# Performance work log

Measured on AMD Instinct MI355X. Metric: run time of the kernel, lower is better.

Reference implementation:

```python
import jax, jax.numpy as jnp
import numpy as np

N, E, F_IN, E_IN, H, L, C = 50000, 500000, 128, 16, 128, 2, 2
BN_EPS = 1e-5


def _linear_params(key, fan_in, fan_out):
    k1, k2 = jax.random.split(key)
    w = jax.random.normal(k1, (fan_in, fan_out), jnp.float32) * (1.0 / np.sqrt(fan_in))
    b = jax.random.normal(k2, (fan_out,), jnp.float32) * 0.01
    return w, b


def setup_inputs() -> dict:
    key = jax.random.key(0)
    ks = jax.random.split(key, 32)
    x = jax.random.normal(ks[0], (N, F_IN), jnp.float32)
    edge_attr = jax.random.normal(ks[1], (E, E_IN), jnp.float32)
    edge_index = jax.random.randint(ks[2], (2, E), 0, N, jnp.int64)

    node_w, node_b = _linear_params(ks[3], F_IN, H)
    edge_w, edge_b = _linear_params(ks[4], E_IN, H)

    def stack(fn, base):
        ws, bs = zip(*[fn(jax.random.fold_in(ks[base], i)) for i in range(L)])
        return jnp.stack(ws), jnp.stack(bs)

    conv_w1, conv_b1 = stack(lambda k: _linear_params(k, H, H), 5)
    conv_w2, conv_b2 = stack(lambda k: _linear_params(k, H, H), 6)
    emlp_w1, emlp_b1 = stack(lambda k: _linear_params(k, 3 * H, H), 7)
    emlp_w2, emlp_b2 = stack(lambda k: _linear_params(k, H, H), 8)
    bn_gamma = jnp.ones((L, H), jnp.float32)
    bn_beta = jnp.zeros((L, H), jnp.float32)

    mlp_w1, mlp_b1 = _linear_params(ks[9], 3 * H, 50)
    mlp_w2, mlp_b2 = _linear_params(ks[10], 50, 25)
    mlp_w3, mlp_b3 = _linear_params(ks[11], 25, C)

    return dict(x=x, edge_attr=edge_attr,
                node_w=node_w, node_b=node_b, edge_w=edge_w, edge_b=edge_b,
                conv_w1=conv_w1, conv_b1=conv_b1, conv_w2=conv_w2, conv_b2=conv_b2,
                bn_gamma=bn_gamma, bn_beta=bn_beta,
                emlp_w1=emlp_w1, emlp_b1=emlp_b1, emlp_w2=emlp_w2, emlp_b2=emlp_b2,
                mlp_w1=mlp_w1, mlp_b1=mlp_b1, mlp_w2=mlp_w2, mlp_b2=mlp_b2,
                mlp_w3=mlp_w3, mlp_b3=mlp_b3, edge_index=edge_index)


def _forward(x, edge_attr, node_w, node_b, edge_w, edge_b,
             conv_w1, conv_b1, conv_w2, conv_b2, bn_gamma, bn_beta,
             emlp_w1, emlp_b1, emlp_w2, emlp_b2,
             mlp_w1, mlp_b1, mlp_w2, mlp_b2, mlp_w3, mlp_b3, edge_index):
    src, dst = edge_index[0], edge_index[1]
    h = x @ node_w + node_b                      # [N, H]
    ea = edge_attr @ edge_w + edge_b             # [E, H]
    for i in range(L):
        # GINEConv: message = relu(x_src + edge_attr), scatter-add at dst
        msg = jax.nn.relu(h[src] + ea)           # [E, H]
        agg = jax.ops.segment_sum(msg, dst, num_segments=N)
        z = h + agg                              # eps = 0
        z = jax.nn.relu(z @ conv_w1[i] + conv_b1[i]) @ conv_w2[i] + conv_b2[i]
        # BatchNorm (training-mode batch statistics over nodes)
        mu = jnp.mean(z, axis=0)
        var = jnp.var(z, axis=0)
        z = bn_gamma[i] * (z - mu) * jax.lax.rsqrt(var + BN_EPS) + bn_beta[i]
        h = (h + jax.nn.relu(z)) * 0.5
        # edge update MLP
        eu = jnp.concatenate([h[src], h[dst], ea], axis=-1)  # [E, 3H]
        ea = ea + (jax.nn.relu(eu @ emlp_w1[i] + emlp_b1[i]) @ emlp_w2[i] + emlp_b2[i]) * 0.5
    # readout: x[edge_index.T].reshape(-1, 2H) cat edge_attr -> [E, 3H]
    feat = jnp.concatenate([h[src], h[dst], ea], axis=-1)
    o = jax.nn.relu(feat @ mlp_w1 + mlp_b1)      # dropout is eval no-op
    o = jax.nn.relu(o @ mlp_w2 + mlp_b2)
    return o @ mlp_w3 + mlp_b3                   # [E, n_classes]


def reference(x, edge_attr, node_w, node_b, edge_w, edge_b,
              conv_w1, conv_b1, conv_w2, conv_b2, bn_gamma, bn_beta,
              emlp_w1, emlp_b1, emlp_w2, emlp_b2,
              mlp_w1, mlp_b1, mlp_w2, mlp_b2, mlp_w3, mlp_b3, edge_index):
    return _forward(x, edge_attr, node_w, node_b, edge_w, edge_b,
                    conv_w1, conv_b1, conv_w2, conv_b2, bn_gamma, bn_beta,
                    emlp_w1, emlp_b1, emlp_w2, emlp_b2,
                    mlp_w1, mlp_b1, mlp_w2, mlp_b2, mlp_w3, mlp_b3, edge_index)
```

## Files before the change

kernel.cpp:

```cpp
#include <hip/hip_runtime.h>


#define NN 50000
#define NE 500000
#define HD 128

typedef _Float16 f16;
typedef _Float16 f16x8 __attribute__((ext_vector_type(8)));
typedef _Float16 f16x4 __attribute__((ext_vector_type(4)));
typedef _Float16 f16x2 __attribute__((ext_vector_type(2)));
typedef float f32x4 __attribute__((ext_vector_type(4)));
typedef unsigned short ushort_t;

#define MFMA16(a, b, c) __builtin_amdgcn_mfma_f32_16x16x32_f16((a), (b), (c), 0, 0, 0)

#define P_NODE_W 0
#define P_NODE_B 16384
#define P_EDGE_W 16512
#define P_EDGE_B 18560
#define P_CONV_W1 18688
#define P_CONV_B1 51456
#define P_CONV_W2 51712
#define P_CONV_B2 84480
#define P_GAMMA 84736
#define P_BETA 84992
#define P_EMLP_W1 85248
#define P_EMLP_B1 183552
#define P_EMLP_W2 183808
#define P_EMLP_B2 216576
#define P_MLP_W1 216832
#define P_MLP_B1 236032
#define P_MLP_W2 236082
#define P_MLP_B2 237332
#define P_MLP_W3 237357
#define P_MLP_B3 237407
#define P_TOTAL 237409

__device__ __forceinline__ float bf2f(unsigned short u) {
    union { unsigned int i; float f; } v;
    v.i = ((unsigned int)u) << 16;
    return v.f;
}

__global__ __launch_bounds__(256) void k_detect(
    const unsigned int* nw, const int* ei, int* flags) {
    __shared__ int cF, cI;
    if (threadIdx.x == 0) { cF = 0; cI = 0; }
    __syncthreads();
    unsigned int u = nw[threadIdx.x];
    int e = (int)((u >> 7) & 0xFFu);
    int odd = ei[2 * threadIdx.x + 1];
    if (e >= 100 && e <= 140) atomicAdd(&cF, 1);
    if (odd != 0) atomicAdd(&cI, 1);
    __syncthreads();
    if (threadIdx.x == 0) {
        flags[0] = (cF < 160) ? 1 : 0;
        flags[1] = (cI < 64) ? 1 : 0;
    }
}

__global__ __launch_bounds__(256) void k_cvt(
    const void* src, f16* dst, int n4, const int* flags) {
    int i = blockIdx.x * 256 + threadIdx.x;
    if (i >= n4) return;
    f16x4 o;
    if (flags[0]) {
        float4 v = ((const float4*)src)[i];
        o[0] = (f16)v.x; o[1] = (f16)v.y; o[2] = (f16)v.z; o[3] = (f16)v.w;
    } else {
        ushort4 v = ((const ushort4*)src)[i];
        o[0] = (f16)bf2f(v.x); o[1] = (f16)bf2f(v.y);
        o[2] = (f16)bf2f(v.z); o[3] = (f16)bf2f(v.w);
    }
    ((f16x4*)dst)[i] = o;
}

__global__ __launch_bounds__(256) void k_cvt_prm(
    const void* p0, const void* p1, const void* p2, const void* p3,
    const void* p4, const void* p5, const void* p6, const void* p7,
    const void* p8, const void* p9, const void* p10, const void* p11,
    const void* p12, const void* p13, const void* p14, const void* p15,
    const void* p16, const void* p17, const void* p18, const void* p19,
    float* prm, const int* flags) {
    int i = blockIdx.x * 256 + threadIdx.x;
    if (i >= P_TOTAL) return;
    const int offs[21] = {P_NODE_W, P_NODE_B, P_EDGE_W, P_EDGE_B, P_CONV_W1,
                          P_CONV_B1, P_CONV_W2, P_CONV_B2, P_GAMMA, P_BETA,
                          P_EMLP_W1, P_EMLP_B1, P_EMLP_W2, P_EMLP_B2, P_MLP_W1,
                          P_MLP_B1, P_MLP_W2, P_MLP_B2, P_MLP_W3, P_MLP_B3,
                          P_TOTAL};
    const void* srcs[20] = {p0, p1, p2, p3, p4, p5, p6, p7, p8, p9, p10, p11,
                            p12, p13, p14, p15, p16, p17, p18, p19};
    int s = 0;
#pragma unroll
    for (int k = 1; k < 20; ++k)
        if (i >= offs[k]) s = k;
    int li = i - offs[s];
    float v = flags[0] ? ((const float*)srcs[s])[li]
                       : bf2f(((const ushort_t*)srcs[s])[li]);
    prm[i] = v;
}

__global__ __launch_bounds__(256) void k_cvt_idx(
    const int* src, int* dst, const int* flags) {
    int i = blockIdx.x * 256 + threadIdx.x;
    if (i >= 2 * NE) return;
    dst[i] = flags[1] ? src[2 * i] : src[i];
}

__global__ __launch_bounds__(256) void k_hist(const int* eix, int* cnt) {
    int e = blockIdx.x * 256 + threadIdx.x;
    if (e < NE) atomicAdd(&cnt[eix[NE + e]], 1);
}

__global__ __launch_bounds__(256) void k_scanA(const int* cnt, int* bsum) {
    __shared__ int wsum[4];
    int tid = threadIdx.x;
    int i = blockIdx.x * 256 + tid;
    int v = (i < NN) ? cnt[i] : 0;
#pragma unroll
    for (int s = 1; s < 64; s <<= 1) v += __shfl_xor(v, s);
    if ((tid & 63) == 0) wsum[tid >> 6] = v;
    __syncthreads();
    if (tid == 0) bsum[blockIdx.x] = wsum[0] + wsum[1] + wsum[2] + wsum[3];
}

__global__ __launch_bounds__(256) void k_scanB(const int* bsum, int* bpre, int* off) {
    __shared__ int l[200];
    int tid = threadIdx.x;
    if (tid < 196) l[tid] = bsum[tid];
    __syncthreads();
    if (tid == 0) {
        int run = 0;
        for (int b = 0; b < 196; ++b) { int t = l[b]; l[b] = run; run += t; }
        off[NN] = run;
    }
    __syncthreads();
    if (tid < 196) bpre[tid] = l[tid];
}

__global__ __launch_bounds__(256) void k_scanC(
    const int* cnt, const int* bpre, int* off, int* cursor) {
    __shared__ int wsum[4];
    int tid = threadIdx.x;
    int lane = tid & 63, wave = tid >> 6;
    int i = blockIdx.x * 256 + tid;
    int v = (i < NN) ? cnt[i] : 0;
    int incl = v;
#pragma unroll
    for (int s = 1; s < 64; s <<= 1) {
        int t = __shfl_up(incl, s);
        if (lane >= s) incl += t;
    }
    if (lane == 63) wsum[wave] = incl;
    __syncthreads();
    int add = bpre[blockIdx.x];
    for (int w = 0; w < 4; ++w)
        if (w < wave) add += wsum[w];
    int excl = add + incl - v;
    if (i < NN) { off[i] = excl; cursor[i] = excl; }
}

__global__ __launch_bounds__(256) void k_scatter(
    const int* eix, int* cursor, int* eord) {
    int e = blockIdx.x * 256 + threadIdx.x;
    if (e >= NE) return;
    int d = eix[NE + e];
    int pos = atomicAdd(&cursor[d], 1);
    eord[pos] = e;
}

__global__ __launch_bounds__(256) void k_gidx(
    const int* eix, const int* eord, int* ssrc, int* sdst) {
    int i = blockIdx.x * 256 + threadIdx.x;
    if (i >= NE) return;
    int e = eord[i];
    ssrc[i] = eix[e];
    sdst[i] = eix[NE + e];
}

__global__ __launch_bounds__(256) void k_agg(
    const f16* ea, const f16* h16, const int* ssrc, const int* off, f16* agg16) {
    int wid = (blockIdx.x * 256 + threadIdx.x) >> 6;
    int lane = threadIdx.x & 63;
    int beg = off[wid], end = off[wid + 1];
    float a0 = 0.f, a1 = 0.f;
    for (int i = beg; i < end; ++i) {
        int s = ssrc[i];
        f16x2 ev = *(const f16x2*)(ea + (size_t)i * HD + lane * 2);
        f16x2 hv = *(const f16x2*)(h16 + (size_t)s * HD + lane * 2);
        a0 += fmaxf((float)ev[0] + (float)hv[0], 0.f);
        a1 += fmaxf((float)ev[1] + (float)hv[1], 0.f);
    }
    f16x2 o; o[0] = (f16)a0; o[1] = (f16)a1;
    *(f16x2*)(agg16 + (size_t)wid * HD + lane * 2) = o;
}

__global__ __launch_bounds__(256) void k_prep(const float* prm, f16* wbuf) {
    int gid = blockIdx.x * 256 + threadIdx.x;
    if (gid < 13 * 16384) {
        int seg = gid >> 14;
        int idx = gid & 16383;
        int off;
        switch (seg) {
            case 0: off = P_NODE_W; break;
            case 1: off = P_CONV_W1; break;
            case 2: off = P_CONV_W1 + 16384; break;
            case 3: off = P_CONV_W2; break;
            case 4: off = P_CONV_W2 + 16384; break;
            case 5: case 6: case 7: off = P_EMLP_W1 + (seg - 5) * 16384; break;
            case 8: case 9: case 10: off = P_EMLP_W1 + 49152 + (seg - 8) * 16384; break;
            case 11: off = P_EMLP_W2; break;
            default: off = P_EMLP_W2 + 16384; break;
        }
        int fb = idx >> 9;
        int sub = (idx & 511) >> 3;
        int j = idx & 7;
        int q = sub >> 4, n = sub & 15;
        int nt = fb >> 2, kt = fb & 3;
        int k = kt * 32 + q * 8 + j;
        int c = nt * 16 + n;
        wbuf[gid] = (f16)prm[off + k * 128 + c];
    } else {
        int t = gid - 13 * 16384;
        if (t >= 3 * 8192) return;
        int s = t >> 13;
        int idx = t & 8191;
        int fb = idx >> 9;
        int sub = (idx & 511) >> 3;
        int j = idx & 7;
        int q = sub >> 4, n = sub & 15;
        int nt = fb >> 2, kt = fb & 3;
        int k = s * 128 + kt * 32 + q * 8 + j;
        int c = nt * 16 + n;
        float v = (c < 50) ? prm[P_MLP_W1 + k * 50 + c] : 0.f;
        wbuf[13 * 16384 + s * 8192 + idx] = (f16)v;
    }
}

__global__ __launch_bounds__(256) void k_node_lin(
    const f16* xc, const f16* wT, const float* bias, f16* h_f16) {
    __shared__ __align__(16) f16 wlds[16384];
    int tid = threadIdx.x;
    {
        const uint4* s = (const uint4*)wT;
        uint4* d = (uint4*)wlds;
        for (int i = tid; i < 2048; i += 256) d[i] = s[i];
    }
    __syncthreads();
    int wave = tid >> 6, lane = tid & 63, q = lane >> 4, ln = lane & 15;
    int rowbase = blockIdx.x * 128 + wave * 32;
    f32x4 acc[2][8] = {};
#pragma unroll
    for (int kt = 0; kt < 4; ++kt) {
        int koff = kt * 32 + q * 8;
        f16x8 a[2];
#pragma unroll
        for (int mt = 0; mt < 2; ++mt) {
            int row = min(rowbase + mt * 16 + ln, NN - 1);
            a[mt] = *(const f16x8*)(xc + row * HD + koff);
        }
#pragma unroll
        for (int nt = 0; nt < 8; ++nt) {
            f16x8 b = *(const f16x8*)&wlds[(nt * 4 + kt) * 512 + lane * 8];
            acc[0][nt] = MFMA16(a[0], b, acc[0][nt]);
            acc[1][nt] = MFMA16(a[1], b, acc[1][nt]);
        }
    }
#pragma unroll
    for (int nt = 0; nt < 8; ++nt) {
        int col = nt * 16 + ln;
        float bv = bias[col];
#pragma unroll
        for (int mt = 0; mt < 2; ++mt)
#pragma unroll
            for (int r = 0; r < 4; ++r) {
                int row = rowbase + mt * 16 + q * 4 + r;
                if (row < NN) h_f16[row * HD + col] = (f16)(acc[mt][nt][r] + bv);
            }
    }
}

__global__ __launch_bounds__(256) void k_edge_lin(
    const f16* eattr, const float* ew, const float* ebias, const int* eord,
    f16* ea) {
    __shared__ float wl[16 * 128];
    __shared__ float bl[128];
    __shared__ float al[64 * 16];
    int tid = threadIdx.x;
    int eb = blockIdx.x * 64;
    for (int i = tid; i < 2048; i += 256) wl[i] = ew[i];
    if (tid < 128) bl[tid] = ebias[tid];
    {
        int e_l = tid >> 2, k0 = (tid & 3) * 4;
        int er = eord[min(eb + e_l, NE - 1)];
        f16x4 u = *(const f16x4*)(eattr + er * 16 + k0);
        al[e_l * 16 + k0 + 0] = (float)u[0];
        al[e_l * 16 + k0 + 1] = (float)u[1];
        al[e_l * 16 + k0 + 2] = (float)u[2];
        al[e_l * 16 + k0 + 3] = (float)u[3];
    }
    __syncthreads();
    for (int i = 0; i < 32; ++i) {
        int o = i * 256 + tid;
        int e_l = o >> 7, c = o & 127;
        float s = bl[c];
#pragma unroll
        for (int k = 0; k < 16; ++k) s += al[e_l * 16 + k] * wl[k * 128 + c];
        int e = eb + e_l;
        if (e < NE) ea[(size_t)e * HD + c] = (f16)s;
    }
}

__global__ __launch_bounds__(256) void k_conv1(
    const f16* h16, const f16* agg16, const f16* wT, const float* bias,
    f16* t_node) {
    __shared__ __align__(16) f16 wlds[16384];
    int tid = threadIdx.x;
    {
        const uint4* s = (const uint4*)wT;
        uint4* d = (uint4*)wlds;
        for (int i = tid; i < 2048; i += 256) d[i] = s[i];
    }
    __syncthreads();
    int wave = tid >> 6, lane = tid & 63, q = lane >> 4, ln = lane & 15;
    int rowbase = blockIdx.x * 128 + wave * 32;
    f32x4 acc[2][8] = {};
#pragma unroll
    for (int kt = 0; kt < 4; ++kt) {
        int koff = kt * 32 + q * 8;
        f16x8 a[2];
#pragma unroll
        for (int mt = 0; mt < 2; ++mt) {
            int row = min(rowbase + mt * 16 + ln, NN - 1);
            f16x8 hv = *(const f16x8*)(h16 + row * HD + koff);
            f16x8 gv = *(const f16x8*)(agg16 + row * HD + koff);
            f16x8 av;
#pragma unroll
            for (int j = 0; j < 8; ++j) av[j] = (f16)((float)hv[j] + (float)gv[j]);
            a[mt] = av;
        }
#pragma unroll
        for (int nt = 0; nt < 8; ++nt) {
            f16x8 b = *(const f16x8*)&wlds[(nt * 4 + kt) * 512 + lane * 8];
            acc[0][nt] = MFMA16(a[0], b, acc[0][nt]);
            acc[1][nt] = MFMA16(a[1], b, acc[1][nt]);
        }
    }
#pragma unroll
    for (int nt = 0; nt < 8; ++nt) {
        int col = nt * 16 + ln;
        float bv = bias[col];
#pragma unroll
        for (int mt = 0; mt < 2; ++mt)
#pragma unroll
            for (int r = 0; r < 4; ++r) {
                int row = rowbase + mt * 16 + q * 4 + r;
                if (row < NN)
                    t_node[row * HD + col] = (f16)fmaxf(acc[mt][nt][r] + bv, 0.f);
            }
    }
}

__global__ __launch_bounds__(256) void k_conv2(
    const f16* t_node, const f16* wT, const float* bias, f16* z2, float* stats) {
    __shared__ __align__(16) f16 wlds[16384];
    int tid = threadIdx.x;
    {
        const uint4* s = (const uint4*)wT;
        uint4* d = (uint4*)wlds;
        for (int i = tid; i < 2048; i += 256) d[i] = s[i];
    }
    __syncthreads();
    int wave = tid >> 6, lane = tid & 63, q = lane >> 4, ln = lane & 15;
    int rowbase = blockIdx.x * 128 + wave * 32;
    f32x4 acc[2][8] = {};
#pragma unroll
    for (int kt = 0; kt < 4; ++kt) {
        int koff = kt * 32 + q * 8;
        f16x8 a[2];
#pragma unroll
        for (int mt = 0; mt < 2; ++mt) {
            int row = min(rowbase + mt * 16 + ln, NN - 1);
            a[mt] = *(const f16x8*)(t_node + row * HD + koff);
        }
#pragma unroll
        for (int nt = 0; nt < 8; ++nt) {
            f16x8 b = *(const f16x8*)&wlds[(nt * 4 + kt) * 512 + lane * 8];
            acc[0][nt] = MFMA16(a[0], b, acc[0][nt]);
            acc[1][nt] = MFMA16(a[1], b, acc[1][nt]);
        }
    }
#pragma unroll
    for (int nt = 0; nt < 8; ++nt) {
        int col = nt * 16 + ln;
        float bv = bias[col];
        float s = 0.f, s2 = 0.f;
#pragma unroll
        for (int mt = 0; mt < 2; ++mt)
#pragma unroll
            for (int r = 0; r < 4; ++r) {
                int row = rowbase + mt * 16 + q * 4 + r;
                if (row < NN) {
                    float v = acc[mt][nt][r] + bv;
                    z2[row * HD + col] = (f16)v;
                    s += v;
                    s2 += v * v;
                }
            }
        s += __shfl_xor(s, 16);  s += __shfl_xor(s, 32);
        s2 += __shfl_xor(s2, 16); s2 += __shfl_xor(s2, 32);
        if (lane < 16) {
            atomicAdd(&stats[col], s);
            atomicAdd(&stats[HD + col], s2);
        }
    }
}

__global__ __launch_bounds__(256) void k_bn(
    const f16* z2, const float* stats, const float* gamma, const float* beta,
    f16* h16) {
    int gid = blockIdx.x * 256 + threadIdx.x;
    if (gid >= NN * HD / 4) return;
    int base = gid * 4;
    int c0 = base & (HD - 1);
    f16x4 z = *(const f16x4*)(z2 + base);
    f16x4 h = *(const f16x4*)(h16 + base);
    f16x4 ho;
#pragma unroll
    for (int j = 0; j < 4; ++j) {
        int c = c0 + j;
        float mu = stats[c] * (1.0f / NN);
        float var = stats[HD + c] * (1.0f / NN) - mu * mu;
        float zn = gamma[c] * ((float)z[j] - mu) * rsqrtf(var + 1e-5f) + beta[c];
        ho[j] = (f16)(((float)h[j] + fmaxf(zn, 0.f)) * 0.5f);
    }
    *(f16x4*)(h16 + base) = ho;
}

__global__ __launch_bounds__(256, 4) void k_emlp(
    const f16* h16, const int* ssrc, const int* sdst, const f16* w1T,
    const float* b1, const f16* w2T, const float* b2, f16* ea) {
    __shared__ __align__(16) f16 wlds[16384];
    int tid = threadIdx.x;
    int eb = blockIdx.x * 128;
    int wave = tid >> 6, lane = tid & 63, q = lane >> 4, ln = lane & 15;
    int g0 = min(eb + wave * 32 + ln, NE - 1);
    int g1 = min(eb + wave * 32 + 16 + ln, NE - 1);
    int is0 = ssrc[g0], is1 = ssrc[g1];
    int id0 = sdst[g0], id1 = sdst[g1];
    f32x4 acc[2][8] = {};
    for (int seg = 0; seg < 3; ++seg) {
        __syncthreads();
        {
            const uint4* s = (const uint4*)(w1T + seg * 16384);
            uint4* d = (uint4*)wlds;
            for (int i = tid; i < 2048; i += 256) d[i] = s[i];
        }
        __syncthreads();
        const f16 *p0, *p1;
        if (seg == 0) {
            p0 = h16 + (size_t)is0 * HD;
            p1 = h16 + (size_t)is1 * HD;
        } else if (seg == 1) {
            p0 = h16 + (size_t)id0 * HD;
            p1 = h16 + (size_t)id1 * HD;
        } else {
            p0 = ea + (size_t)g0 * HD;
            p1 = ea + (size_t)g1 * HD;
        }
        f16x8 f0[4], f1[4];
#pragma unroll
        for (int kt = 0; kt < 4; ++kt) {
            f0[kt] = *(const f16x8*)(p0 + kt * 32 + q * 8);
            f1[kt] = *(const f16x8*)(p1 + kt * 32 + q * 8);
        }
#pragma unroll
        for (int kt = 0; kt < 4; ++kt)
#pragma unroll
            for (int mt = 0; mt < 8; ++mt) {
                f16x8 a = *(const f16x8*)&wlds[(mt * 4 + kt) * 512 + lane * 8];
                acc[0][mt] = MFMA16(a, f0[kt], acc[0][mt]);
                acc[1][mt] = MFMA16(a, f1[kt], acc[1][mt]);
            }
    }
    union HU { f16 h; unsigned short u; };
    unsigned int pk[2][4][4];
#pragma unroll
    for (int ntl = 0; ntl < 2; ++ntl)
#pragma unroll
        for (int kt = 0; kt < 4; ++kt) {
            f32x4 blo = *(const f32x4*)(b1 + (2 * kt) * 16 + q * 4);
            f32x4 bhi = *(const f32x4*)(b1 + (2 * kt + 1) * 16 + q * 4);
#pragma unroll
            for (int r = 0; r < 4; ++r) {
                HU lo, hi;
                lo.h = (f16)fmaxf(acc[ntl][2 * kt][r] + blo[r], 0.f);
                hi.h = (f16)fmaxf(acc[ntl][2 * kt + 1][r] + bhi[r], 0.f);
                pk[ntl][kt][r] =
                    (unsigned int)lo.u | ((unsigned int)hi.u << 16);
            }
        }
    __syncthreads();
    {
        const uint4* s = (const uint4*)w2T;
        uint4* d = (uint4*)wlds;
        for (int i = tid; i < 2048; i += 256) d[i] = s[i];
    }
    __syncthreads();
    int s1 = (((2 * q) & 3) << 4) | ln;
    int s2 = (((2 * q + 1) & 3) << 4) | ln;
    int hsh = (q >> 1) * 16;
    f32x4 acc2[2][8] = {};
#pragma unroll
    for (int kt = 0; kt < 4; ++kt) {
        f16x8 bf[2];
#pragma unroll
        for (int ntl = 0; ntl < 2; ++ntl) {
            union { unsigned short u[8]; f16x8 v; } bb;
#pragma unroll
            for (int r = 0; r < 4; ++r) {
                unsigned int v1 = (unsigned int)__shfl((int)pk[ntl][kt][r], s1);
                unsigned int v2 = (unsigned int)__shfl((int)pk[ntl][kt][r], s2);
                bb.u[r] = (unsigned short)(v1 >> hsh);
                bb.u[4 + r] = (unsigned short)(v2 >> hsh);
            }
            bf[ntl] = bb.v;
        }
#pragma unroll
        for (int mt = 0; mt < 8; ++mt) {
            f16x8 a = *(const f16x8*)&wlds[(mt * 4 + kt) * 512 + lane * 8];
            acc2[0][mt] = MFMA16(a, bf[0], acc2[0][mt]);
            acc2[1][mt] = MFMA16(a, bf[1], acc2[1][mt]);
        }
    }
#pragma unroll
    for (int ntl = 0; ntl < 2; ++ntl) {
        int e = eb + wave * 32 + ntl * 16 + ln;
        if (e < NE) {
            f16* erow = ea + (size_t)e * HD;
#pragma unroll
            for (int mt = 0; mt < 8; ++mt) {
                int c0 = mt * 16 + q * 4;
                f32x4 bv = *(const f32x4*)(b2 + c0);
                f16x4 old = *(const f16x4*)(erow + c0);
                f16x4 nw;
#pragma unroll
                for (int r = 0; r < 4; ++r)
                    nw[r] = (f16)((float)old[r] +
                                  0.5f * (acc2[ntl][mt][r] + bv[r]));
                *(f16x4*)(erow + c0) = nw;
            }
        }
    }
}

__global__ __launch_bounds__(256) void k_readout(
    const f16* h16, const f16* ea, const int* ssrc, const int* sdst,
    const int* eord, const f16* w1Tp, const float* mb1, const float* mw2,
    const float* mb2, const float* mw3, const float* mb3, float* out) {
    __shared__ __align__(16) f16 wlds[8192];
    __shared__ f16 o1[256 * 58];
    __shared__ float w2l[50 * 28];
    __shared__ float w3l[50];
    __shared__ float b2l[25];
    __shared__ float b3l[2];
    __shared__ int sidx[256], didx[256];
    int tid = threadIdx.x;
    int eb = blockIdx.x * 256;
    {
        int e = min(eb + tid, NE - 1);
        sidx[tid] = ssrc[e];
        didx[tid] = sdst[e];
    }
    for (int i = tid; i < 50 * 28; i += 256) {
        int k = i / 28, ko = i - k * 28;
        w2l[i] = (ko < 25) ? mw2[k * 25 + ko] : 0.f;
    }
    if (tid < 50) w3l[tid] = mw3[tid];
    if (tid < 25) b2l[tid] = mb2[tid];
    if (tid < 2) b3l[tid] = mb3[tid];
    int wave = tid >> 6, lane = tid & 63, q = lane >> 4, ln = lane & 15;
    f32x4 acc[4][4] = {};
    for (int seg = 0; seg < 3; ++seg) {
        __syncthreads();
        {
            const uint4* s = (const uint4*)(w1Tp + seg * 8192);
            uint4* d = (uint4*)wlds;
            for (int i = tid; i < 1024; i += 256) d[i] = s[i];
        }
        __syncthreads();
#pragma unroll
        for (int kt = 0; kt < 4; ++kt) {
            int koff = kt * 32 + q * 8;
            f16x8 a[4];
#pragma unroll
            for (int mt = 0; mt < 4; ++mt) {
                int le = wave * 64 + mt * 16 + ln;
                const f16* ap;
                if (seg == 0)      ap = h16 + (size_t)sidx[le] * HD + koff;
                else if (seg == 1) ap = h16 + (size_t)didx[le] * HD + koff;
                else               ap = ea + (size_t)min(eb + le, NE - 1) * HD + koff;
                a[mt] = *(const f16x8*)ap;
            }
#pragma unroll
            for (int nt = 0; nt < 4; ++nt) {
                f16x8 b = *(const f16x8*)&wlds[(nt * 4 + kt) * 512 + lane * 8];
#pragma unroll
                for (int mt = 0; mt < 4; ++mt)
                    acc[mt][nt] = MFMA16(a[mt], b, acc[mt][nt]);
            }
        }
    }
#pragma unroll
    for (int nt = 0; nt < 4; ++nt) {
        int col = nt * 16 + ln;
        if (col < 50) {
            float bv = mb1[col];
#pragma unroll
            for (int mt = 0; mt < 4; ++mt)
#pragma unroll
                for (int r = 0; r < 4; ++r) {
                    int le = wave * 64 + mt * 16 + q * 4 + r;
                    o1[le * 58 + col] = (f16)fmaxf(acc[mt][nt][r] + bv, 0.f);
                }
        }
    }
    __syncthreads();
    float o2[25];
#pragma unroll
    for (int ko = 0; ko < 25; ++ko) o2[ko] = b2l[ko];
    for (int k = 0; k < 50; ++k) {
        float a = (float)o1[tid * 58 + k];
#pragma unroll
        for (int ko = 0; ko < 25; ++ko) o2[ko] += a * w2l[k * 28 + ko];
    }
    float r0 = b3l[0], r1 = b3l[1];
#pragma unroll
    for (int ko = 0; ko < 25; ++ko) {
        float a = fmaxf(o2[ko], 0.f);
        r0 += a * w3l[ko * 2];
        r1 += a * w3l[ko * 2 + 1];
    }
    int e = eb + tid;
    if (e < NE) {
        int oe = eord[e];
        float2 o; o.x = r0; o.y = r1;
        *(float2*)(out + (size_t)oe * 2) = o;
    }
}

extern "C" void kernel_launch(void* const* d_in, const int* in_sizes, int n_in,
                              void* d_out, int out_size, void* d_ws, size_t ws_size,
                              hipStream_t stream) {
    const size_t WS_NEED = 197425936ULL;
    if (ws_size < WS_NEED) {
        hipMemsetAsync(d_out, 0, (size_t)out_size * 4, stream);
        return;
    }
    char* ws = (char*)d_ws;
    f16* ea = (f16*)(ws);
    f16* hf16 = (f16*)(ws + 128000000LL);
    f16* agg16 = (f16*)(ws + 140800000LL);
    f16* xc = (f16*)(ws + 140800000LL);
    int* eord = (int*)(ws + 153600000LL);
    int* off = (int*)(ws + 155600000LL);
    int* cntcur = (int*)(ws + 155800064LL);
    int* bsum = (int*)(ws + 156000064LL);
    int* bpre = (int*)(ws + 156001088LL);
    int* ssrc = (int*)(ws + 156002176LL);
    int* sdst = (int*)(ws + 158002176LL);
    f16* eattr16 = (f16*)(ws + 166400000LL);
    f16* z2 = (f16*)(ws + 166400000LL);
    f16* tn = (f16*)(ws + 179200000LL);
    f16* wbuf = (f16*)(ws + 192000000LL);
    float* stats = (float*)(ws + 192475136LL);
    float* prm = (float*)(ws + 192476160LL);
    int* eix = (int*)(ws + 193425920LL);
    int* flags = (int*)(ws + 197425920LL);
    float* out = (float*)d_out;

    k_detect<<<1, 256, 0, stream>>>((const unsigned int*)d_in[2],
                                    (const int*)d_in[22], flags);
    k_cvt<<<6250, 256, 0, stream>>>(d_in[0], xc, 1600000, flags);
    k_cvt<<<7813, 256, 0, stream>>>(d_in[1], eattr16, 2000000, flags);
    k_cvt_prm<<<928, 256, 0, stream>>>(
        d_in[2], d_in[3], d_in[4], d_in[5], d_in[6], d_in[7], d_in[8], d_in[9],
        d_in[10], d_in[11], d_in[12], d_in[13], d_in[14], d_in[15], d_in[16],
        d_in[17], d_in[18], d_in[19], d_in[20], d_in[21], prm, flags);
    k_cvt_idx<<<3907, 256, 0, stream>>>((const int*)d_in[22], eix, flags);

    hipMemsetAsync(cntcur, 0, NN * 4, stream);
    k_hist<<<1954, 256, 0, stream>>>(eix, cntcur);
    k_scanA<<<196, 256, 0, stream>>>(cntcur, bsum);
    k_scanB<<<1, 256, 0, stream>>>(bsum, bpre, off);
    k_scanC<<<196, 256, 0, stream>>>(cntcur, bpre, off, cntcur);
    k_scatter<<<1954, 256, 0, stream>>>(eix, cntcur, eord);
    k_gidx<<<1954, 256, 0, stream>>>(eix, eord, ssrc, sdst);

    k_prep<<<928, 256, 0, stream>>>(prm, wbuf);
    k_node_lin<<<391, 256, 0, stream>>>(xc, wbuf, prm + P_NODE_B, hf16);
    k_edge_lin<<<7813, 256, 0, stream>>>(eattr16, prm + P_EDGE_W, prm + P_EDGE_B,
                                         eord, ea);

    for (int l = 0; l < 2; ++l) {
        hipMemsetAsync(stats, 0, 1024, stream);
        k_agg<<<12500, 256, 0, stream>>>(ea, hf16, ssrc, off, agg16);
        k_conv1<<<391, 256, 0, stream>>>(hf16, agg16, wbuf + (1 + l) * 16384,
                                         prm + P_CONV_B1 + l * HD, tn);
        k_conv2<<<391, 256, 0, stream>>>(tn, wbuf + (3 + l) * 16384,
                                         prm + P_CONV_B2 + l * HD, z2, stats);
        k_bn<<<6250, 256, 0, stream>>>(z2, stats, prm + P_GAMMA + l * HD,
                                       prm + P_BETA + l * HD, hf16);
        k_emlp<<<3907, 256, 0, stream>>>(hf16, ssrc, sdst,
                                         wbuf + (5 + l * 3) * 16384,
                                         prm + P_EMLP_B1 + l * HD,
                                         wbuf + (11 + l) * 16384,
                                         prm + P_EMLP_B2 + l * HD, ea);
    }
    k_readout<<<1954, 256, 0, stream>>>(hf16, ea, ssrc, sdst, eord,
                                        wbuf + 13 * 16384,
                                        prm + P_MLP_B1, prm + P_MLP_W2,
                                        prm + P_MLP_B2, prm + P_MLP_W3,
                                        prm + P_MLP_B3, out);
}
```

Baseline: 966.4 us.

## Make edge MLP kernel persistent with all weights resident in LDS

Changes k_emlp to a persistent kernel with 256 blocks of 1024 threads. Each block loads both layer weight matrices (128 KB of f16) into shared memory once, then each wave loops over 32-edge tiles. This removes the repeated per-block weight staging and the __syncthreads barriers between segments. The cost is one 1024-thread block per CU, since 128 KB of LDS leaves little room for more, and waves get no cross-block latency hiding for the gathered loads.

```diff
diff --git a/kernel.cpp b/kernel.cpp
--- a/kernel.cpp
+++ b/kernel.cpp
@@ -438,118 +438,120 @@
     *(f16x4*)(h16 + base) = ho;
 }
 
-__global__ __launch_bounds__(256, 4) void k_emlp(
-    const f16* h16, const int* ssrc, const int* sdst, const f16* w1T,
-    const float* b1, const f16* w2T, const float* b2, f16* ea) {
-    __shared__ __align__(16) f16 wlds[16384];
-    int tid = threadIdx.x;
-    int eb = blockIdx.x * 128;
+__global__ __launch_bounds__(1024, 4) void k_emlp(
+    const f16* __restrict__ h16, const int* __restrict__ ssrc,
+    const int* __restrict__ sdst, const f16* __restrict__ w1T,
+    const float* __restrict__ b1, const f16* __restrict__ w2T,
+    const float* __restrict__ b2, f16* __restrict__ ea) {
+    __shared__ __align__(16) f16 wlds[65536];
+    int tid = threadIdx.x;
+    {
+        const uint4* s1 = (const uint4*)w1T;
+        uint4* d = (uint4*)wlds;
+        for (int i = tid; i < 6144; i += 1024) d[i] = s1[i];
+        const uint4* s2 = (const uint4*)w2T;
+        uint4* d2 = (uint4*)(wlds + 49152);
+        for (int i = tid; i < 2048; i += 1024) d2[i] = s2[i];
+    }
+    __syncthreads();
     int wave = tid >> 6, lane = tid & 63, q = lane >> 4, ln = lane & 15;
-    int g0 = min(eb + wave * 32 + ln, NE - 1);
-    int g1 = min(eb + wave * 32 + 16 + ln, NE - 1);
-    int is0 = ssrc[g0], is1 = ssrc[g1];
-    int id0 = sdst[g0], id1 = sdst[g1];
-    f32x4 acc[2][8] = {};
-    for (int seg = 0; seg < 3; ++seg) {
-        __syncthreads();
-        {
-            const uint4* s = (const uint4*)(w1T + seg * 16384);
-            uint4* d = (uint4*)wlds;
-            for (int i = tid; i < 2048; i += 256) d[i] = s[i];
-        }
-        __syncthreads();
-        const f16 *p0, *p1;
-        if (seg == 0) {
-            p0 = h16 + (size_t)is0 * HD;
-            p1 = h16 + (size_t)is1 * HD;
-        } else if (seg == 1) {
-            p0 = h16 + (size_t)id0 * HD;
-            p1 = h16 + (size_t)id1 * HD;
-        } else {
-            p0 = ea + (size_t)g0 * HD;
-            p1 = ea + (size_t)g1 * HD;
-        }
-        f16x8 f0[4], f1[4];
+    int sh1 = (((2 * q) & 3) << 4) | ln;
+    int sh2 = (((2 * q + 1) & 3) << 4) | ln;
+    int hsh = (q >> 1) * 16;
+    const int NT = (NE + 31) / 32;
+    for (int t = blockIdx.x * 16 + wave; t < NT; t += 256 * 16) {
+        int eb32 = t * 32;
+        int g0 = min(eb32 + ln, NE - 1);
+        int g1 = min(eb32 + 16 + ln, NE - 1);
+        int is0 = ssrc[g0], is1 = ssrc[g1];
+        int id0 = sdst[g0], id1 = sdst[g1];
+        f32x4 acc[2][8] = {};
+#pragma unroll
+        for (int seg = 0; seg < 3; ++seg) {
+            const f16 *p0, *p1;
+            if (seg == 0) {
+                p0 = h16 + (size_t)is0 * HD;
+                p1 = h16 + (size_t)is1 * HD;
+            } else if (seg == 1) {
+                p0 = h16 + (size_t)id0 * HD;
+                p1 = h16 + (size_t)id1 * HD;
+            } else {
+                p0 = ea + (size_t)g0 * HD;
+                p1 = ea + (size_t)g1 * HD;
+            }
+            f16x8 f0[4], f1[4];
+#pragma unroll
+            for (int kt = 0; kt < 4; ++kt) {
+                f0[kt] = *(const f16x8*)(p0 + kt * 32 + q * 8);
+                f1[kt] = *(const f16x8*)(p1 + kt * 32 + q * 8);
+            }
+#pragma unroll
+            for (int kt = 0; kt < 4; ++kt)
+#pragma unroll
+                for (int mt = 0; mt < 8; ++mt) {
+                    f16x8 a = *(const f16x8*)&wlds[seg * 16384 +
+                                                   (mt * 4 + kt) * 512 + lane * 8];
+                    acc[0][mt] = MFMA16(a, f0[kt], acc[0][mt]);
+                    acc[1][mt] = MFMA16(a, f1[kt], acc[1][mt]);
+                }
+        }
+        union HU { f16 h; unsigned short u; };
+        unsigned int pk[2][4][4];
+#pragma unroll
+        for (int ntl = 0; ntl < 2; ++ntl)
+#pragma unroll
+            for (int kt = 0; kt < 4; ++kt) {
+                f32x4 blo = *(const f32x4*)(b1 + (2 * kt) * 16 + q * 4);
+                f32x4 bhi = *(const f32x4*)(b1 + (2 * kt + 1) * 16 + q * 4);
+#pragma unroll
+                for (int r = 0; r < 4; ++r) {
+                    HU lo, hi;
+                    lo.h = (f16)fmaxf(acc[ntl][2 * kt][r] + blo[r], 0.f);
+                    hi.h = (f16)fmaxf(acc[ntl][2 * kt + 1][r] + bhi[r], 0.f);
+                    pk[ntl][kt][r] =
+                        (unsigned int)lo.u | ((unsigned int)hi.u << 16);
+                }
+            }
+        f32x4 acc2[2][8] = {};
 #pragma unroll
         for (int kt = 0; kt < 4; ++kt) {
-            f0[kt] = *(const f16x8*)(p0 + kt * 32 + q * 8);
-            f1[kt] = *(const f16x8*)(p1 + kt * 32 + q * 8);
-        }
-#pragma unroll
-        for (int kt = 0; kt < 4; ++kt)
+            f16x8 bf[2];
+#pragma unroll
+            for (int ntl = 0; ntl < 2; ++ntl) {
+                union { unsigned short u[8]; f16x8 v; } bb;
+#pragma unroll
+                for (int r = 0; r < 4; ++r) {
+                    unsigned int v1 = (unsigned int)__shfl((int)pk[ntl][kt][r], sh1);
+                    unsigned int v2 = (unsigned int)__shfl((int)pk[ntl][kt][r], sh2);
+                    bb.u[r] = (unsigned short)(v1 >> hsh);
+                    bb.u[4 + r] = (unsigned short)(v2 >> hsh);
+                }
+                bf[ntl] = bb.v;
+            }
 #pragma unroll
             for (int mt = 0; mt < 8; ++mt) {
-                f16x8 a = *(const f16x8*)&wlds[(mt * 4 + kt) * 512 + lane * 8];
-                acc[0][mt] = MFMA16(a, f0[kt], acc[0][mt]);
-                acc[1][mt] = MFMA16(a, f1[kt], acc[1][mt]);
-            }
-    }
-    union HU { f16 h; unsigned short u; };
-    unsigned int pk[2][4][4];
-#pragma unroll
-    for (int ntl = 0; ntl < 2; ++ntl)
-#pragma unroll
-        for (int kt = 0; kt < 4; ++kt) {
-            f32x4 blo = *(const f32x4*)(b1 + (2 * kt) * 16 + q * 4);
-            f32x4 bhi = *(const f32x4*)(b1 + (2 * kt + 1) * 16 + q * 4);
-#pragma unroll
-            for (int r = 0; r < 4; ++r) {
-                HU lo, hi;
-                lo.h = (f16)fmaxf(acc[ntl][2 * kt][r] + blo[r], 0.f);
-                hi.h = (f16)fmaxf(acc[ntl][2 * kt + 1][r] + bhi[r], 0.f);
-                pk[ntl][kt][r] =
-                    (unsigned int)lo.u | ((unsigned int)hi.u << 16);
-            }
-        }
-    __syncthreads();
-    {
-        const uint4* s = (const uint4*)w2T;
-        uint4* d = (uint4*)wlds;
-        for (int i = tid; i < 2048; i += 256) d[i] = s[i];
-    }
-    __syncthreads();
-    int s1 = (((2 * q) & 3) << 4) | ln;
-    int s2 = (((2 * q + 1) & 3) << 4) | ln;
-    int hsh = (q >> 1) * 16;
-    f32x4 acc2[2][8] = {};
-#pragma unroll
-    for (int kt = 0; kt < 4; ++kt) {
-        f16x8 bf[2];
+                f16x8 a = *(const f16x8*)&wlds[49152 + (mt * 4 + kt) * 512 + lane * 8];
+                acc2[0][mt] = MFMA16(a, bf[0], acc2[0][mt]);
+                acc2[1][mt] = MFMA16(a, bf[1], acc2[1][mt]);
+            }
+        }
 #pragma unroll
         for (int ntl = 0; ntl < 2; ++ntl) {
-            union { unsigned short u[8]; f16x8 v; } bb;
-#pragma unroll
-            for (int r = 0; r < 4; ++r) {
-                unsigned int v1 = (unsigned int)__shfl((int)pk[ntl][kt][r], s1);
-                unsigned int v2 = (unsigned int)__shfl((int)pk[ntl][kt][r], s2);
-                bb.u[r] = (unsigned short)(v1 >> hsh);
-                bb.u[4 + r] = (unsigned short)(v2 >> hsh);
-            }
-            bf[ntl] = bb.v;
-        }
-#pragma unroll
-        for (int mt = 0; mt < 8; ++mt) {
-            f16x8 a = *(const f16x8*)&wlds[(mt * 4 + kt) * 512 + lane * 8];
-            acc2[0][mt] = MFMA16(a, bf[0], acc2[0][mt]);
-            acc2[1][mt] = MFMA16(a, bf[1], acc2[1][mt]);
-        }
-    }
-#pragma unroll
-    for (int ntl = 0; ntl < 2; ++ntl) {
-        int e = eb + wave * 32 + ntl * 16 + ln;
-        if (e < NE) {
-            f16* erow = ea + (size_t)e * HD;
-#pragma unroll
-            for (int mt = 0; mt < 8; ++mt) {
-                int c0 = mt * 16 + q * 4;
-                f32x4 bv = *(const f32x4*)(b2 + c0);
-                f16x4 old = *(const f16x4*)(erow + c0);
-                f16x4 nw;
-#pragma unroll
-                for (int r = 0; r < 4; ++r)
-                    nw[r] = (f16)((float)old[r] +
-                                  0.5f * (acc2[ntl][mt][r] + bv[r]));
-                *(f16x4*)(erow + c0) = nw;
+            int e = eb32 + ntl * 16 + ln;
+            if (e < NE) {
+                f16* erow = ea + (size_t)e * HD;
+#pragma unroll
+                for (int mt = 0; mt < 8; ++mt) {
+                    int c0 = mt * 16 + q * 4;
+                    f32x4 bv = *(const f32x4*)(b2 + c0);
+                    f16x4 old = *(const f16x4*)(erow + c0);
+                    f16x4 nw;
+#pragma unroll
+                    for (int r = 0; r < 4; ++r)
+                        nw[r] = (f16)((float)old[r] +
+                                      0.5f * (acc2[ntl][mt][r] + bv[r]));
+                    *(f16x4*)(erow + c0) = nw;
+                }
             }
         }
     }
@@ -712,7 +714,7 @@
                                          prm + P_CONV_B2 + l * HD, z2, stats);
         k_bn<<<6250, 256, 0, stream>>>(z2, stats, prm + P_GAMMA + l * HD,
                                        prm + P_BETA + l * HD, hf16);
-        k_emlp<<<3907, 256, 0, stream>>>(hf16, ssrc, sdst,
+        k_emlp<<<256, 1024, 0, stream>>>(hf16, ssrc, sdst,
                                          wbuf + (5 + l * 3) * 16384,
                                          prm + P_EMLP_B1 + l * HD,
                                          wbuf + (11 + l) * 16384,
```

Measured after the change: 2.315 ms. +139.6%, slower.
